# Optimization experiments

Hardware: AMD Instinct MI355X
Metric: run time of the kernel (lower is better)

The kernel has to match this reference:

```python
import jax, jax.numpy as jnp
import numpy as np

N = 50000        # nodes
E = 800000       # directed edges (before self-loops)
NODE_DIM = 128
HIDDEN = 64
HEADS = 4
C = HIDDEN // HEADS   # 16 per-head channels
LAYERS = 4
G = 256          # graphs in batch
EPS = 1e-5       # BatchNorm eps
SLOPE = 0.2      # GAT leaky_relu negative slope


def setup_inputs() -> dict:
    key = jax.random.key(0)
    ks = jax.random.split(key, 12)

    def gl(k, shape, fan_in):  # glorot-ish init
        return jax.random.normal(k, shape, jnp.float32) * np.float32(1.0 / np.sqrt(fan_in))

    x = jax.random.normal(ks[0], (N, NODE_DIM), jnp.float32)
    edge_index = jax.random.randint(ks[1], (2, E), 0, N)
    batch = jnp.sort(jax.random.randint(ks[2], (N,), 0, G))

    return {
        "x": x,
        "embed_W": gl(ks[3], (NODE_DIM, HIDDEN), NODE_DIM),
        "embed_b": jnp.zeros((HIDDEN,), jnp.float32),
        "gat_W": gl(ks[4], (LAYERS, HIDDEN, HIDDEN), HIDDEN),
        "att_src": gl(ks[5], (LAYERS, HEADS, C), C),
        "att_dst": gl(ks[6], (LAYERS, HEADS, C), C),
        "gat_b": jnp.zeros((LAYERS, HIDDEN), jnp.float32),
        "bn_gamma": jnp.ones((LAYERS, HIDDEN), jnp.float32),
        "bn_beta": jnp.zeros((LAYERS, HIDDEN), jnp.float32),
        "fc1_W": gl(ks[7], (HIDDEN, HIDDEN), HIDDEN),
        "fc1_b": jnp.zeros((HIDDEN,), jnp.float32),
        "fc2_W": gl(ks[8], (HIDDEN, 1), HIDDEN),
        "fc2_b": jnp.zeros((1,), jnp.float32),
        "edge_index": edge_index,
        "batch": batch,
    }


def reference(x, embed_W, embed_b, gat_W, att_src, att_dst, gat_b,
              bn_gamma, bn_beta, fc1_W, fc1_b, fc2_W, fc2_b,
              edge_index, batch):
    # GATConv default: add self-loops (message flows src -> dst)
    loops = jnp.arange(N)
    src = jnp.concatenate([edge_index[0], loops])
    dst = jnp.concatenate([edge_index[1], loops])

    h = x @ embed_W + embed_b  # [N, HIDDEN]
    for l in range(LAYERS):
        xp = (h @ gat_W[l]).reshape(N, HEADS, C)          # per-head transform
        a_s = jnp.sum(xp * att_src[l], axis=-1)           # [N, H]
        a_d = jnp.sum(xp * att_dst[l], axis=-1)           # [N, H]
        e = jax.nn.leaky_relu(a_s[src] + a_d[dst], SLOPE) # [E', H]
        # segment softmax over incoming edges of each dst node
        m = jax.ops.segment_max(e, dst, num_segments=N)
        p = jnp.exp(e - m[dst])
        s = jax.ops.segment_sum(p, dst, num_segments=N)
        alpha = p / (s[dst] + 1e-16)                      # [E', H]
        msg = xp[src] * alpha[:, :, None]                 # [E', H, C]
        h = jax.ops.segment_sum(msg, dst, num_segments=N).reshape(N, HIDDEN) + gat_b[l]
        # BatchNorm over nodes (training-mode batch stats, biased variance)
        mu = jnp.mean(h, axis=0)
        var = jnp.var(h, axis=0)
        h = (h - mu) * jax.lax.rsqrt(var + EPS) * bn_gamma[l] + bn_beta[l]
        h = jax.nn.elu(h)

    g = jax.ops.segment_sum(h, batch, num_segments=G)     # global_add_pool
    g = jax.nn.relu(g @ fc1_W + fc1_b)                    # dropout: identity (eval)
    return (g @ fc2_W + fc2_b).reshape(-1)                # [G]
```

## Files before the change

kernel.cpp:

```cpp
#include <hip/hip_runtime.h>

#define N_NODES 50000
#define N_EDGES 800000
#define NODE_DIM 128
#define HIDDEN 64
#define HEADS 4
#define LAYERS 4
#define NGRAPH 256
#define BN_EPS 1e-5f
#define SLOPE 0.2f
#define NTILES 196
#define BN_BLOCKS 256
#define NPW 16

typedef unsigned short u16;
typedef unsigned int   u32;

__device__ __forceinline__ float b2f(u16 v) { return __uint_as_float(((u32)v) << 16); }
__device__ __forceinline__ u16 f2b(float f) {
    u32 u = __float_as_uint(f);
    u32 r = (u + 0x7FFFu + ((u >> 16) & 1u)) >> 16;
    return (u16)r;
}
__device__ __forceinline__ float ld(const void* p, int i, int isf) {
    return isf ? ((const float*)p)[i] : b2f(((const u16*)p)[i]);
}

__global__ void k_mark(u16* out, u16 pat) { out[threadIdx.x] = pat; }

__global__ void k_init(const void* gamma, int* flag, int* cnt) {
    int i = blockIdx.x * 256 + threadIdx.x;
    if (i < N_NODES) cnt[i] = 0;
    if (i == 0) *flag = (((const u32*)gamma)[0] == 0x3F800000u) ? 1 : 0;
}

__global__ void k_count(const int* __restrict__ ei, int* __restrict__ cnt,
                        int* __restrict__ eslot) {
    int e = blockIdx.x * 256 + threadIdx.x;
    if (e >= N_EDGES) return;
    eslot[e] = atomicAdd(&cnt[ei[N_EDGES + e]], 1);
}
__global__ void k_scan1(const int* __restrict__ cnt, int* __restrict__ row_ptr,
                        int* __restrict__ tsum) {
    int b = blockIdx.x, t = threadIdx.x, i = b * 256 + t;
    int c = (i < N_NODES) ? cnt[i] : 0;
    __shared__ int ps[256];
    ps[t] = c;
    __syncthreads();
    for (int off = 1; off < 256; off <<= 1) {
        int v = (t >= off) ? ps[t - off] : 0;
        __syncthreads();
        ps[t] += v;
        __syncthreads();
    }
    if (i < N_NODES) row_ptr[i] = ps[t] - c;
    if (t == 255) tsum[b] = ps[255];
}
__global__ void k_scan3(int* __restrict__ row_ptr, const int* __restrict__ tsum) {
    __shared__ int ps[256];
    int t = threadIdx.x;
    int c = (t < NTILES) ? tsum[t] : 0;
    ps[t] = c;
    __syncthreads();
    for (int off = 1; off < 256; off <<= 1) {
        int v = (t >= off) ? ps[t - off] : 0;
        __syncthreads();
        ps[t] += v;
        __syncthreads();
    }
    int toff_b = (blockIdx.x == 0) ? 0 : ps[blockIdx.x - 1];
    int i = blockIdx.x * 256 + t;
    if (i < N_NODES) row_ptr[i] += toff_b;
    if (i == 0) row_ptr[N_NODES] = N_EDGES;
}
__global__ void k_fill(const int* __restrict__ ei, const int* __restrict__ row_ptr,
                       const int* __restrict__ eslot, int* __restrict__ col) {
    int e = blockIdx.x * 256 + threadIdx.x;
    if (e >= N_EDGES) return;
    col[row_ptr[ei[N_EDGES + e]] + eslot[e]] = ei[e];
}

template<int ISF>
__device__ __forceinline__ void embed_tr_body(const void* __restrict__ x,
                                              const void* __restrict__ W,
                                              const void* __restrict__ b,
                                              const void* __restrict__ W0,
                                              const void* __restrict__ asrc,
                                              const void* __restrict__ adst,
                                              u16* __restrict__ xp16,
                                              float* __restrict__ a_s,
                                              float* __restrict__ a_d,
                                              float* __restrict__ bn_part) {
    int t = threadIdx.x;
    int n0 = blockIdx.x * NPW;
    if (blockIdx.x < BN_BLOCKS) {
        bn_part[blockIdx.x * 128 + t] = 0.f;
        bn_part[blockIdx.x * 128 + 64 + t] = 0.f;
    }
    __shared__ float xs[2][4][NODE_DIM];
    __shared__ float hbuf[NPW][HIDDEN];

    {
        float wreg[NODE_DIM];
#pragma unroll
        for (int k = 0; k < NODE_DIM; k++) wreg[k] = ld(W, k * HIDDEN + t, ISF);
        float bias = ld(b, t, ISF);

        float2 r[4];
#pragma unroll
        for (int i = 0; i < 4; i++) {
            if (ISF) {
                r[i] = ((const float2*)x)[(size_t)(n0 + i) * (NODE_DIM / 2) + t];
            } else {
                u32 v = ((const u32*)x)[(size_t)(n0 + i) * (NODE_DIM / 2) + t];
                r[i] = make_float2(__uint_as_float(v << 16), __uint_as_float(v & 0xFFFF0000u));
            }
        }
#pragma unroll
        for (int i = 0; i < 4; i++) *(float2*)&xs[0][i][2 * t] = r[i];

        for (int g = 0; g < NPW / 4; g++) {
            float2 rn[4];
            if (g + 1 < NPW / 4) {
#pragma unroll
                for (int i = 0; i < 4; i++) {
                    int n = n0 + (g + 1) * 4 + i;
                    if (ISF) {
                        rn[i] = ((const float2*)x)[(size_t)n * (NODE_DIM / 2) + t];
                    } else {
                        u32 v = ((const u32*)x)[(size_t)n * (NODE_DIM / 2) + t];
                        rn[i] = make_float2(__uint_as_float(v << 16),
                                            __uint_as_float(v & 0xFFFF0000u));
                    }
                }
            }
#pragma unroll
            for (int i = 0; i < 4; i++) {
                const float* xr = xs[g & 1][i];
                float a0 = 0.f, a1 = 0.f, a2 = 0.f, a3 = 0.f;
#pragma unroll
                for (int k = 0; k < NODE_DIM; k += 4) {
                    float4 xv = *(const float4*)&xr[k];
                    a0 += xv.x * wreg[k];
                    a1 += xv.y * wreg[k + 1];
                    a2 += xv.z * wreg[k + 2];
                    a3 += xv.w * wreg[k + 3];
                }
                hbuf[g * 4 + i][t] = (a0 + a1) + (a2 + a3) + bias;
            }
            if (g + 1 < NPW / 4) {
#pragma unroll
                for (int i = 0; i < 4; i++) *(float2*)&xs[(g + 1) & 1][i][2 * t] = rn[i];
            }
        }
    }

    float w0[HIDDEN];
#pragma unroll
    for (int k = 0; k < HIDDEN; k++) w0[k] = ld(W0, k * HIDDEN + t, ISF);
    float vsc = ld(asrc, t, ISF);
    float vdc = ld(adst, t, ISF);

#pragma unroll 2
    for (int i = 0; i < NPW; i++) {
        int n = n0 + i;
        const float* hr = hbuf[i];
        float a0 = 0.f, a1 = 0.f, a2 = 0.f, a3 = 0.f;
#pragma unroll
        for (int k = 0; k < HIDDEN; k += 4) {
            float4 xv = *(const float4*)&hr[k];
            a0 += xv.x * w0[k];
            a1 += xv.y * w0[k + 1];
            a2 += xv.z * w0[k + 2];
            a3 += xv.w * w0[k + 3];
        }
        float acc = (a0 + a1) + (a2 + a3);
        xp16[(size_t)n * HIDDEN + t] = f2b(acc);
        float vs = acc * vsc, vd = acc * vdc;
#pragma unroll
        for (int o = 1; o < 16; o <<= 1) {
            vs += __shfl_xor(vs, o, 16);
            vd += __shfl_xor(vd, o, 16);
        }
        if ((t & 15) == 0) {
            a_s[n * HEADS + (t >> 4)] = vs;
            a_d[n * HEADS + (t >> 4)] = vd;
        }
    }
}
__global__ void __launch_bounds__(64)
k_embed_tr(const void* __restrict__ x, const void* __restrict__ W,
           const void* __restrict__ b, const void* __restrict__ W0,
           const void* __restrict__ asrc, const void* __restrict__ adst,
           const int* __restrict__ fl,
           u16* __restrict__ xp16, float* __restrict__ a_s, float* __restrict__ a_d,
           float* __restrict__ bn_part) {
    if (*fl) embed_tr_body<1>(x, W, b, W0, asrc, adst, xp16, a_s, a_d, bn_part);
    else     embed_tr_body<0>(x, W, b, W0, asrc, adst, xp16, a_s, a_d, bn_part);
}

template<int ISF>
__device__ __forceinline__ void transform_body(const float* __restrict__ h,
                                               const void* __restrict__ W,
                                               const void* __restrict__ asrc,
                                               const void* __restrict__ adst, int l,
                                               const float* __restrict__ bnss,
                                               u16* __restrict__ xp16,
                                               float* __restrict__ a_s,
                                               float* __restrict__ a_d,
                                               float* __restrict__ bn_part) {
    int t = threadIdx.x;
    int n0 = blockIdx.x * NPW;
    if (blockIdx.x < BN_BLOCKS) {
        bn_part[blockIdx.x * 128 + t] = 0.f;
        bn_part[blockIdx.x * 128 + 64 + t] = 0.f;
    }
    __shared__ float hsb[2][4][HIDDEN];
    float wreg[HIDDEN];
#pragma unroll
    for (int k = 0; k < HIDDEN; k++) wreg[k] = ld(W, l * HIDDEN * HIDDEN + k * HIDDEN + t, ISF);
    float vsc = ld(asrc, l * HIDDEN + t, ISF);
    float vdc = ld(adst, l * HIDDEN + t, ISF);
    float sc = bnss[t], sh = bnss[64 + t];

    float r[4];
#pragma unroll
    for (int i = 0; i < 4; i++) {
        float v = h[(size_t)(n0 + i) * HIDDEN + t];
        v = v * sc + sh;
        v = v > 0.f ? v : (__expf(v) - 1.f);
        r[i] = v;
    }
#pragma unroll
    for (int i = 0; i < 4; i++) hsb[0][i][t] = r[i];

    for (int g = 0; g < NPW / 4; g++) {
        float rn[4];
        if (g + 1 < NPW / 4) {
#pragma unroll
            for (int i = 0; i < 4; i++)
                rn[i] = h[(size_t)(n0 + (g + 1) * 4 + i) * HIDDEN + t];
        }
#pragma unroll
        for (int i = 0; i < 4; i++) {
            int n = n0 + g * 4 + i;
            const float* hr = hsb[g & 1][i];
            float a0 = 0.f, a1 = 0.f, a2 = 0.f, a3 = 0.f;
#pragma unroll
            for (int k = 0; k < HIDDEN; k += 4) {
                float4 xv = *(const float4*)&hr[k];
                a0 += xv.x * wreg[k];
                a1 += xv.y * wreg[k + 1];
                a2 += xv.z * wreg[k + 2];
                a3 += xv.w * wreg[k + 3];
            }
            float acc = (a0 + a1) + (a2 + a3);
            xp16[(size_t)n * HIDDEN + t] = f2b(acc);
            float vs = acc * vsc, vd = acc * vdc;
#pragma unroll
            for (int o = 1; o < 16; o <<= 1) {
                vs += __shfl_xor(vs, o, 16);
                vd += __shfl_xor(vd, o, 16);
            }
            if ((t & 15) == 0) {
                a_s[n * HEADS + (t >> 4)] = vs;
                a_d[n * HEADS + (t >> 4)] = vd;
            }
        }
        if (g + 1 < NPW / 4) {
#pragma unroll
            for (int i = 0; i < 4; i++) {
                float v = rn[i];
                v = v * sc + sh;
                v = v > 0.f ? v : (__expf(v) - 1.f);
                hsb[(g + 1) & 1][i][t] = v;
            }
        }
    }
}
__global__ void __launch_bounds__(64)
k_transform(const float* __restrict__ h, const void* __restrict__ W,
            const void* __restrict__ asrc, const void* __restrict__ adst,
            const int* __restrict__ fl, int l,
            const float* __restrict__ bnss,
            u16* __restrict__ xp16, float* __restrict__ a_s,
            float* __restrict__ a_d, float* __restrict__ bn_part) {
    if (*fl) transform_body<1>(h, W, asrc, adst, l, bnss, xp16, a_s, a_d, bn_part);
    else     transform_body<0>(h, W, asrc, adst, l, bnss, xp16, a_s, a_d, bn_part);
}

__global__ void __launch_bounds__(256)
k_gather(const int* __restrict__ row_ptr, const int* __restrict__ col,
         const float* __restrict__ a_s, const float* __restrict__ a_d,
         const u16* __restrict__ xp16, float* __restrict__ h,
         float* __restrict__ bn_part) {
    int d = blockIdx.x * 4 + (threadIdx.x >> 6);
    int t = threadIdx.x & 63;
    int hd = t >> 4, l16 = t & 15, hb = hd << 4;
    int beg = row_ptr[d], end = row_ptr[d + 1];
    float ad = a_d[d * HEADS + hd];

    float m = a_s[d * HEADS + hd] + ad;
    m = m > 0.f ? m : SLOPE * m;
    float s = 1.f;
    float acc = b2f(xp16[(size_t)d * HIDDEN + t]);

    for (int j0 = beg; j0 < end; j0 += 16) {
        int jj = j0 + l16;
        int sv = col[jj < end ? jj : end - 1];
        float e = -1e30f;
        if (jj < end) {
            e = a_s[sv * HEADS + hd] + ad;
            e = e > 0.f ? e : SLOPE * e;
        }
        float cm = e;
#pragma unroll
        for (int o = 1; o < 16; o <<= 1) cm = fmaxf(cm, __shfl_xor(cm, o, 16));
        float nm = fmaxf(m, cm);
        float scale = __expf(m - nm);
        float alpha = (jj < end) ? __expf(e - nm) : 0.f;
        float cs = alpha;
#pragma unroll
        for (int o = 1; o < 16; o <<= 1) cs += __shfl_xor(cs, o, 16);
        s = s * scale + cs;
        acc *= scale;
#pragma unroll
        for (int q = 0; q < 16; q++) {
            int   svq = __shfl(sv, q, 64);
            float aq  = __shfl(alpha, hb + q, 64);
            acc += aq * b2f(xp16[(size_t)svq * HIDDEN + t]);
        }
        m = nm;
    }
    float v = acc / (s + 1e-16f);
    h[(size_t)d * HIDDEN + t] = v;

    __shared__ float s1[256];
    __shared__ float s2[256];
    s1[threadIdx.x] = v;
    s2[threadIdx.x] = v * v;
    __syncthreads();
    if (threadIdx.x < 64) {
        float su = s1[t] + s1[64 + t] + s1[128 + t] + s1[192 + t];
        float sq = s2[t] + s2[64 + t] + s2[128 + t] + s2[192 + t];
        float* bp = bn_part + (blockIdx.x & (BN_BLOCKS - 1)) * 128;
        atomicAdd(bp + t, su);
        atomicAdd(bp + 64 + t, sq);
    }
}

__global__ void k_bn_final(const float* __restrict__ bn_part,
                           const void* __restrict__ gamma, const void* __restrict__ beta,
                           const int* __restrict__ fl, int l, float* __restrict__ bnss) {
    int t = threadIdx.x;
    float sum = 0.f, sq = 0.f;
#pragma unroll 8
    for (int b = 0; b < BN_BLOCKS; b++) {
        sum += bn_part[b * 128 + t];
        sq  += bn_part[b * 128 + 64 + t];
    }
    int isf = *fl;
    const float inv_n = 1.f / (float)N_NODES;
    float mu  = sum * inv_n;
    float var = sq * inv_n - mu * mu;
    float sc = rsqrtf(var + BN_EPS) * ld(gamma, l * HIDDEN + t, isf);
    bnss[t]      = sc;
    bnss[64 + t] = ld(beta, l * HIDDEN + t, isf) - mu * sc;
}

__global__ void __launch_bounds__(1024)
k_poolmlp(const float* __restrict__ h, const int* __restrict__ batch,
          const float* __restrict__ bnss,
          const void* __restrict__ W1, const void* __restrict__ b1,
          const void* __restrict__ W2, const void* __restrict__ b2,
          const int* __restrict__ fl, void* __restrict__ out) {
    int gr = blockIdx.x;
    int t = threadIdx.x & 63, w = threadIdx.x >> 6;
    int lo = 0, hi = N_NODES;
    while (lo < hi) { int mid = (lo + hi) >> 1; if (batch[mid] < gr) lo = mid + 1; else hi = mid; }
    int beg = lo;
    lo = 0; hi = N_NODES;
    while (lo < hi) { int mid = (lo + hi) >> 1; if (batch[mid] < gr + 1) lo = mid + 1; else hi = mid; }
    int end = lo;
    float sc = bnss[t], sh = bnss[64 + t];
    float acc = 0.f;
    for (int n = beg + w; n < end; n += 16) {
        float v = h[(size_t)n * HIDDEN + t] * sc + sh;
        acc += v > 0.f ? v : (__expf(v) - 1.f);
    }
    __shared__ float sd[1024];
    __shared__ float gs[64];
    sd[threadIdx.x] = acc;
    __syncthreads();
    if (w < 8) sd[threadIdx.x] += sd[threadIdx.x + 512];
    __syncthreads();
    if (w < 4) sd[threadIdx.x] += sd[threadIdx.x + 256];
    __syncthreads();
    if (w < 2) sd[threadIdx.x] += sd[threadIdx.x + 128];
    __syncthreads();
    if (w == 0) gs[t] = sd[t] + sd[t + 64];
    __syncthreads();
    if (w == 0) {
        int isf = *fl;
        float a1 = ld(b1, t, isf);
        for (int k = 0; k < HIDDEN; k++) a1 += gs[k] * ld(W1, k * HIDDEN + t, isf);
        a1 = fmaxf(a1, 0.f);
        float p = a1 * ld(W2, t, isf);
#pragma unroll
        for (int o = 1; o < 64; o <<= 1) p += __shfl_xor(p, o, 64);
        if (t == 0) {
            float r = p + ld(b2, 0, isf);
            if (isf) ((float*)out)[gr] = r;
            else     ((u16*)out)[gr]   = f2b(r);
        }
    }
}

extern "C" void kernel_launch(void* const* d_in, const int* in_sizes, int n_in,
                              void* d_out, int out_size, void* d_ws, size_t ws_size,
                              hipStream_t stream) {
    u16* out16 = (u16*)d_out;

    bool sizes_ok = (n_in == 15) && (out_size == NGRAPH)
        && in_sizes[0] == N_NODES * NODE_DIM
        && in_sizes[1] == NODE_DIM * HIDDEN
        && in_sizes[2] == HIDDEN
        && in_sizes[3] == LAYERS * HIDDEN * HIDDEN
        && in_sizes[4] == LAYERS * HIDDEN
        && in_sizes[5] == LAYERS * HIDDEN
        && in_sizes[6] == LAYERS * HIDDEN
        && in_sizes[7] == LAYERS * HIDDEN
        && in_sizes[8] == LAYERS * HIDDEN
        && in_sizes[9] == HIDDEN * HIDDEN
        && in_sizes[10] == HIDDEN
        && in_sizes[11] == HIDDEN
        && in_sizes[12] == 1
        && in_sizes[13] == 2 * N_EDGES
        && in_sizes[14] == N_NODES;
    if (!sizes_ok) { k_mark<<<1, 256, 0, stream>>>(out16, 0x4442); return; }

    float* ws      = (float*)d_ws;
    float* h       = ws;
    u16*   xp16    = (u16*)(ws + 3200000);
    float* a_s     = ws + 4800000;
    float* a_d     = ws + 5000000;
    float* bn_part = ws + 5200000;
    float* bnss    = ws + 5232768;
    int* row_ptr   = (int*)(ws + 5232896);
    int* cnt       = row_ptr + 50001;
    int* eslot     = cnt + 50000;
    int* col       = eslot + 800000;
    int* tsum      = col + 800000;
    int* dflag     = tsum + 256;

    const size_t NEED_BYTES =
        (size_t)(5232896 + 50001 + 50000 + 800000 + 800000 + 256 + 1) * 4;
    if (ws_size < NEED_BYTES) { k_mark<<<1, 256, 0, stream>>>(out16, 0x447A); return; }

    const void* x        = d_in[0];
    const void* embed_W  = d_in[1];
    const void* embed_b  = d_in[2];
    const void* gat_W    = d_in[3];
    const void* att_src  = d_in[4];
    const void* att_dst  = d_in[5];
    const void* bn_gamma = d_in[7];
    const void* bn_beta  = d_in[8];
    const void* fc1_W    = d_in[9];
    const void* fc1_b    = d_in[10];
    const void* fc2_W    = d_in[11];
    const void* fc2_b    = d_in[12];
    const int* ei        = (const int*)d_in[13];
    const int* batch     = (const int*)d_in[14];

    const int e_blocks = (N_EDGES + 255) / 256;
    k_init<<<(N_NODES + 255) / 256, 256, 0, stream>>>(bn_gamma, dflag, cnt);
    k_count<<<e_blocks, 256, 0, stream>>>(ei, cnt, eslot);
    k_scan1<<<NTILES, 256, 0, stream>>>(cnt, row_ptr, tsum);
    k_scan3<<<NTILES, 256, 0, stream>>>(row_ptr, tsum);
    k_fill<<<e_blocks, 256, 0, stream>>>(ei, row_ptr, eslot, col);

    k_embed_tr<<<N_NODES / NPW, 64, 0, stream>>>(x, embed_W, embed_b, gat_W,
                                                 att_src, att_dst, dflag,
                                                 xp16, a_s, a_d, bn_part);

    for (int l = 0; l < LAYERS; l++) {
        if (l > 0)
            k_transform<<<N_NODES / NPW, 64, 0, stream>>>(h, gat_W, att_src, att_dst,
                                                          dflag, l, bnss,
                                                          xp16, a_s, a_d, bn_part);
        k_gather<<<N_NODES / 4, 256, 0, stream>>>(row_ptr, col, a_s, a_d, xp16, h, bn_part);
        k_bn_final<<<1, 64, 0, stream>>>(bn_part, bn_gamma, bn_beta, dflag, l, bnss);
    }

    k_poolmlp<<<NGRAPH, 1024, 0, stream>>>(h, batch, bnss, fc1_W, fc1_b, fc2_W, fc2_b,
                                           dflag, d_out);
}
```

Measured before the change: 465.8 us.

## Use lane broadcasts instead of LDS for node transforms; fold BN finalize into gather

The embed and transform kernels now keep node feature rows in registers and broadcast each element with readlane instead of staging rows through shared memory. This removes LDS traffic and the related synchronisation. The separate single-block BN finalize kernel is removed: the gather kernel uses an atomic ticket so the last block computes the BN scale and shift. That saves four kernel launches but adds a grid-wide atomic and threadfences, and readlane runs on the scalar path, which may limit throughput.

```diff
diff --git a/kernel.cpp b/kernel.cpp
--- a/kernel.cpp
+++ b/kernel.cpp
@@ -25,6 +25,9 @@
 __device__ __forceinline__ float ld(const void* p, int i, int isf) {
     return isf ? ((const float*)p)[i] : b2f(((const u16*)p)[i]);
 }
+__device__ __forceinline__ float bcast(float v, int l) {
+    return __uint_as_float((u32)__builtin_amdgcn_readlane((int)__float_as_uint(v), l));
+}
 
 __global__ void k_mark(u16* out, u16 pat) { out[threadIdx.x] = pat; }
 
@@ -78,6 +81,16 @@
     int e = blockIdx.x * 256 + threadIdx.x;
     if (e >= N_EDGES) return;
     col[row_ptr[ei[N_EDGES + e]] + eslot[e]] = ei[e];
+}
+
+template<int ISF>
+__device__ __forceinline__ float2 ldx2(const void* x, int n, int t) {
+    if (ISF) {
+        return ((const float2*)x)[(size_t)n * (NODE_DIM / 2) + t];
+    } else {
+        u32 v = ((const u32*)x)[(size_t)n * (NODE_DIM / 2) + t];
+        return make_float2(__uint_as_float(v << 16), __uint_as_float(v & 0xFFFF0000u));
+    }
 }
 
 template<int ISF>
@@ -90,102 +103,69 @@
                                               u16* __restrict__ xp16,
                                               float* __restrict__ a_s,
                                               float* __restrict__ a_d,
-                                              float* __restrict__ bn_part) {
+                                              float* __restrict__ bn_part,
+                                              int* __restrict__ ticket) {
     int t = threadIdx.x;
     int n0 = blockIdx.x * NPW;
     if (blockIdx.x < BN_BLOCKS) {
         bn_part[blockIdx.x * 128 + t] = 0.f;
         bn_part[blockIdx.x * 128 + 64 + t] = 0.f;
-    }
-    __shared__ float xs[2][4][NODE_DIM];
-    __shared__ float hbuf[NPW][HIDDEN];
-
-    {
-        float wreg[NODE_DIM];
-#pragma unroll
-        for (int k = 0; k < NODE_DIM; k++) wreg[k] = ld(W, k * HIDDEN + t, ISF);
-        float bias = ld(b, t, ISF);
-
-        float2 r[4];
-#pragma unroll
-        for (int i = 0; i < 4; i++) {
-            if (ISF) {
-                r[i] = ((const float2*)x)[(size_t)(n0 + i) * (NODE_DIM / 2) + t];
-            } else {
-                u32 v = ((const u32*)x)[(size_t)(n0 + i) * (NODE_DIM / 2) + t];
-                r[i] = make_float2(__uint_as_float(v << 16), __uint_as_float(v & 0xFFFF0000u));
-            }
-        }
-#pragma unroll
-        for (int i = 0; i < 4; i++) *(float2*)&xs[0][i][2 * t] = r[i];
-
-        for (int g = 0; g < NPW / 4; g++) {
-            float2 rn[4];
-            if (g + 1 < NPW / 4) {
-#pragma unroll
-                for (int i = 0; i < 4; i++) {
-                    int n = n0 + (g + 1) * 4 + i;
-                    if (ISF) {
-                        rn[i] = ((const float2*)x)[(size_t)n * (NODE_DIM / 2) + t];
-                    } else {
-                        u32 v = ((const u32*)x)[(size_t)n * (NODE_DIM / 2) + t];
-                        rn[i] = make_float2(__uint_as_float(v << 16),
-                                            __uint_as_float(v & 0xFFFF0000u));
-                    }
-                }
-            }
-#pragma unroll
-            for (int i = 0; i < 4; i++) {
-                const float* xr = xs[g & 1][i];
-                float a0 = 0.f, a1 = 0.f, a2 = 0.f, a3 = 0.f;
-#pragma unroll
-                for (int k = 0; k < NODE_DIM; k += 4) {
-                    float4 xv = *(const float4*)&xr[k];
-                    a0 += xv.x * wreg[k];
-                    a1 += xv.y * wreg[k + 1];
-                    a2 += xv.z * wreg[k + 2];
-                    a3 += xv.w * wreg[k + 3];
-                }
-                hbuf[g * 4 + i][t] = (a0 + a1) + (a2 + a3) + bias;
-            }
-            if (g + 1 < NPW / 4) {
-#pragma unroll
-                for (int i = 0; i < 4; i++) *(float2*)&xs[(g + 1) & 1][i][2 * t] = rn[i];
-            }
-        }
-    }
-
+        if (blockIdx.x == 0 && t == 0) *ticket = 0;
+    }
+    float wreg[NODE_DIM];
+#pragma unroll
+    for (int k = 0; k < NODE_DIM; k++) wreg[k] = ld(W, k * HIDDEN + t, ISF);
     float w0[HIDDEN];
 #pragma unroll
     for (int k = 0; k < HIDDEN; k++) w0[k] = ld(W0, k * HIDDEN + t, ISF);
+    float bias = ld(b, t, ISF);
     float vsc = ld(asrc, t, ISF);
     float vdc = ld(adst, t, ISF);
 
-#pragma unroll 2
-    for (int i = 0; i < NPW; i++) {
-        int n = n0 + i;
-        const float* hr = hbuf[i];
-        float a0 = 0.f, a1 = 0.f, a2 = 0.f, a3 = 0.f;
-#pragma unroll
-        for (int k = 0; k < HIDDEN; k += 4) {
-            float4 xv = *(const float4*)&hr[k];
-            a0 += xv.x * w0[k];
-            a1 += xv.y * w0[k + 1];
-            a2 += xv.z * w0[k + 2];
-            a3 += xv.w * w0[k + 3];
-        }
-        float acc = (a0 + a1) + (a2 + a3);
-        xp16[(size_t)n * HIDDEN + t] = f2b(acc);
-        float vs = acc * vsc, vd = acc * vdc;
-#pragma unroll
-        for (int o = 1; o < 16; o <<= 1) {
-            vs += __shfl_xor(vs, o, 16);
-            vd += __shfl_xor(vd, o, 16);
-        }
-        if ((t & 15) == 0) {
-            a_s[n * HEADS + (t >> 4)] = vs;
-            a_d[n * HEADS + (t >> 4)] = vd;
-        }
+    float2 r[4], rn[4];
+#pragma unroll
+    for (int i = 0; i < 4; i++) r[i] = ldx2<ISF>(x, n0 + i, t);
+
+    for (int g = 0; g < NPW / 4; g++) {
+        if (g + 1 < NPW / 4) {
+#pragma unroll
+            for (int i = 0; i < 4; i++) rn[i] = ldx2<ISF>(x, n0 + (g + 1) * 4 + i, t);
+        }
+#pragma unroll
+        for (int i = 0; i < 4; i++) {
+            int n = n0 + g * 4 + i;
+            float a0 = 0.f, a1 = 0.f, a2 = 0.f, a3 = 0.f;
+#pragma unroll
+            for (int j = 0; j < 64; j += 2) {
+                a0 = fmaf(bcast(r[i].x, j),     wreg[2 * j],     a0);
+                a1 = fmaf(bcast(r[i].y, j),     wreg[2 * j + 1], a1);
+                a2 = fmaf(bcast(r[i].x, j + 1), wreg[2 * j + 2], a2);
+                a3 = fmaf(bcast(r[i].y, j + 1), wreg[2 * j + 3], a3);
+            }
+            float hv = (a0 + a1) + (a2 + a3) + bias;
+            float c0 = 0.f, c1 = 0.f, c2 = 0.f, c3 = 0.f;
+#pragma unroll
+            for (int j = 0; j < HIDDEN; j += 4) {
+                c0 = fmaf(bcast(hv, j),     w0[j],     c0);
+                c1 = fmaf(bcast(hv, j + 1), w0[j + 1], c1);
+                c2 = fmaf(bcast(hv, j + 2), w0[j + 2], c2);
+                c3 = fmaf(bcast(hv, j + 3), w0[j + 3], c3);
+            }
+            float acc = (c0 + c1) + (c2 + c3);
+            xp16[(size_t)n * HIDDEN + t] = f2b(acc);
+            float vs = acc * vsc, vd = acc * vdc;
+#pragma unroll
+            for (int o = 1; o < 16; o <<= 1) {
+                vs += __shfl_xor(vs, o, 16);
+                vd += __shfl_xor(vd, o, 16);
+            }
+            if ((t & 15) == 0) {
+                a_s[n * HEADS + (t >> 4)] = vs;
+                a_d[n * HEADS + (t >> 4)] = vd;
+            }
+        }
+#pragma unroll
+        for (int i = 0; i < 4; i++) r[i] = rn[i];
     }
 }
 __global__ void __launch_bounds__(64)
@@ -194,9 +174,9 @@
            const void* __restrict__ asrc, const void* __restrict__ adst,
            const int* __restrict__ fl,
            u16* __restrict__ xp16, float* __restrict__ a_s, float* __restrict__ a_d,
-           float* __restrict__ bn_part) {
-    if (*fl) embed_tr_body<1>(x, W, b, W0, asrc, adst, xp16, a_s, a_d, bn_part);
-    else     embed_tr_body<0>(x, W, b, W0, asrc, adst, xp16, a_s, a_d, bn_part);
+           float* __restrict__ bn_part, int* __restrict__ ticket) {
+    if (*fl) embed_tr_body<1>(x, W, b, W0, asrc, adst, xp16, a_s, a_d, bn_part, ticket);
+    else     embed_tr_body<0>(x, W, b, W0, asrc, adst, xp16, a_s, a_d, bn_part, ticket);
 }
 
 template<int ISF>
@@ -208,14 +188,15 @@
                                                u16* __restrict__ xp16,
                                                float* __restrict__ a_s,
                                                float* __restrict__ a_d,
-                                               float* __restrict__ bn_part) {
+                                               float* __restrict__ bn_part,
+                                               int* __restrict__ ticket) {
     int t = threadIdx.x;
     int n0 = blockIdx.x * NPW;
     if (blockIdx.x < BN_BLOCKS) {
         bn_part[blockIdx.x * 128 + t] = 0.f;
         bn_part[blockIdx.x * 128 + 64 + t] = 0.f;
-    }
-    __shared__ float hsb[2][4][HIDDEN];
+        if (blockIdx.x == 0 && t == 0) *ticket = 0;
+    }
     float wreg[HIDDEN];
 #pragma unroll
     for (int k = 0; k < HIDDEN; k++) wreg[k] = ld(W, l * HIDDEN * HIDDEN + k * HIDDEN + t, ISF);
@@ -223,38 +204,32 @@
     float vdc = ld(adst, l * HIDDEN + t, ISF);
     float sc = bnss[t], sh = bnss[64 + t];
 
-    float r[4];
+    float v[4], vn[4];
 #pragma unroll
     for (int i = 0; i < 4; i++) {
-        float v = h[(size_t)(n0 + i) * HIDDEN + t];
-        v = v * sc + sh;
-        v = v > 0.f ? v : (__expf(v) - 1.f);
-        r[i] = v;
-    }
-#pragma unroll
-    for (int i = 0; i < 4; i++) hsb[0][i][t] = r[i];
+        float u = h[(size_t)(n0 + i) * HIDDEN + t];
+        u = u * sc + sh;
+        v[i] = u > 0.f ? u : (__expf(u) - 1.f);
+    }
 
     for (int g = 0; g < NPW / 4; g++) {
-        float rn[4];
         if (g + 1 < NPW / 4) {
 #pragma unroll
             for (int i = 0; i < 4; i++)
-                rn[i] = h[(size_t)(n0 + (g + 1) * 4 + i) * HIDDEN + t];
+                vn[i] = h[(size_t)(n0 + (g + 1) * 4 + i) * HIDDEN + t];
         }
 #pragma unroll
         for (int i = 0; i < 4; i++) {
             int n = n0 + g * 4 + i;
-            const float* hr = hsb[g & 1][i];
-            float a0 = 0.f, a1 = 0.f, a2 = 0.f, a3 = 0.f;
-#pragma unroll
-            for (int k = 0; k < HIDDEN; k += 4) {
-                float4 xv = *(const float4*)&hr[k];
-                a0 += xv.x * wreg[k];
-                a1 += xv.y * wreg[k + 1];
-                a2 += xv.z * wreg[k + 2];
-                a3 += xv.w * wreg[k + 3];
-            }
-            float acc = (a0 + a1) + (a2 + a3);
+            float c0 = 0.f, c1 = 0.f, c2 = 0.f, c3 = 0.f;
+#pragma unroll
+            for (int j = 0; j < HIDDEN; j += 4) {
+                c0 = fmaf(bcast(v[i], j),     wreg[j],     c0);
+                c1 = fmaf(bcast(v[i], j + 1), wreg[j + 1], c1);
+                c2 = fmaf(bcast(v[i], j + 2), wreg[j + 2], c2);
+                c3 = fmaf(bcast(v[i], j + 3), wreg[j + 3], c3);
+            }
+            float acc = (c0 + c1) + (c2 + c3);
             xp16[(size_t)n * HIDDEN + t] = f2b(acc);
             float vs = acc * vsc, vd = acc * vdc;
 #pragma unroll
@@ -270,10 +245,8 @@
         if (g + 1 < NPW / 4) {
 #pragma unroll
             for (int i = 0; i < 4; i++) {
-                float v = rn[i];
-                v = v * sc + sh;
-                v = v > 0.f ? v : (__expf(v) - 1.f);
-                hsb[(g + 1) & 1][i][t] = v;
+                float u = vn[i] * sc + sh;
+                v[i] = u > 0.f ? u : (__expf(u) - 1.f);
             }
         }
     }
@@ -284,16 +257,19 @@
             const int* __restrict__ fl, int l,
             const float* __restrict__ bnss,
             u16* __restrict__ xp16, float* __restrict__ a_s,
-            float* __restrict__ a_d, float* __restrict__ bn_part) {
-    if (*fl) transform_body<1>(h, W, asrc, adst, l, bnss, xp16, a_s, a_d, bn_part);
-    else     transform_body<0>(h, W, asrc, adst, l, bnss, xp16, a_s, a_d, bn_part);
+            float* __restrict__ a_d, float* __restrict__ bn_part,
+            int* __restrict__ ticket) {
+    if (*fl) transform_body<1>(h, W, asrc, adst, l, bnss, xp16, a_s, a_d, bn_part, ticket);
+    else     transform_body<0>(h, W, asrc, adst, l, bnss, xp16, a_s, a_d, bn_part, ticket);
 }
 
 __global__ void __launch_bounds__(256)
 k_gather(const int* __restrict__ row_ptr, const int* __restrict__ col,
          const float* __restrict__ a_s, const float* __restrict__ a_d,
          const u16* __restrict__ xp16, float* __restrict__ h,
-         float* __restrict__ bn_part) {
+         float* __restrict__ bn_part, int* __restrict__ ticket,
+         const void* __restrict__ gamma, const void* __restrict__ beta,
+         const int* __restrict__ fl, int l, float* __restrict__ bnss) {
     int d = blockIdx.x * 4 + (threadIdx.x >> 6);
     int t = threadIdx.x & 63;
     int hd = t >> 4, l16 = t & 15, hb = hd << 4;
@@ -337,6 +313,7 @@
 
     __shared__ float s1[256];
     __shared__ float s2[256];
+    __shared__ int lastBlk;
     s1[threadIdx.x] = v;
     s2[threadIdx.x] = v * v;
     __syncthreads();
@@ -347,25 +324,27 @@
         atomicAdd(bp + t, su);
         atomicAdd(bp + 64 + t, sq);
     }
-}
-
-__global__ void k_bn_final(const float* __restrict__ bn_part,
-                           const void* __restrict__ gamma, const void* __restrict__ beta,
-                           const int* __restrict__ fl, int l, float* __restrict__ bnss) {
-    int t = threadIdx.x;
-    float sum = 0.f, sq = 0.f;
+    if (threadIdx.x == 0) {
+        __threadfence();
+        lastBlk = (atomicAdd(ticket, 1) == (int)gridDim.x - 1);
+    }
+    __syncthreads();
+    if (lastBlk && threadIdx.x < 64) {
+        __threadfence();
+        float sum = 0.f, sq = 0.f;
 #pragma unroll 8
-    for (int b = 0; b < BN_BLOCKS; b++) {
-        sum += bn_part[b * 128 + t];
-        sq  += bn_part[b * 128 + 64 + t];
-    }
-    int isf = *fl;
-    const float inv_n = 1.f / (float)N_NODES;
-    float mu  = sum * inv_n;
-    float var = sq * inv_n - mu * mu;
-    float sc = rsqrtf(var + BN_EPS) * ld(gamma, l * HIDDEN + t, isf);
-    bnss[t]      = sc;
-    bnss[64 + t] = ld(beta, l * HIDDEN + t, isf) - mu * sc;
+        for (int bb = 0; bb < BN_BLOCKS; bb++) {
+            sum += bn_part[bb * 128 + t];
+            sq  += bn_part[bb * 128 + 64 + t];
+        }
+        int isf = *fl;
+        const float inv_n = 1.f / (float)N_NODES;
+        float mu  = sum * inv_n;
+        float var = sq * inv_n - mu * mu;
+        float scl = rsqrtf(var + BN_EPS) * ld(gamma, l * HIDDEN + t, isf);
+        bnss[t]      = scl;
+        bnss[64 + t] = ld(beta, l * HIDDEN + t, isf) - mu * scl;
+    }
 }
 
 __global__ void __launch_bounds__(1024)
@@ -452,9 +431,10 @@
     int* col       = eslot + 800000;
     int* tsum      = col + 800000;
     int* dflag     = tsum + 256;
+    int* ticket    = dflag + 1;
 
     const size_t NEED_BYTES =
-        (size_t)(5232896 + 50001 + 50000 + 800000 + 800000 + 256 + 1) * 4;
+        (size_t)(5232896 + 50001 + 50000 + 800000 + 800000 + 256 + 2) * 4;
     if (ws_size < NEED_BYTES) { k_mark<<<1, 256, 0, stream>>>(out16, 0x447A); return; }
 
     const void* x        = d_in[0];
@@ -481,15 +461,16 @@
 
     k_embed_tr<<<N_NODES / NPW, 64, 0, stream>>>(x, embed_W, embed_b, gat_W,
                                                  att_src, att_dst, dflag,
-                                                 xp16, a_s, a_d, bn_part);
+                                                 xp16, a_s, a_d, bn_part, ticket);
 
     for (int l = 0; l < LAYERS; l++) {
         if (l > 0)
             k_transform<<<N_NODES / NPW, 64, 0, stream>>>(h, gat_W, att_src, att_dst,
                                                           dflag, l, bnss,
-                                                          xp16, a_s, a_d, bn_part);
-        k_gather<<<N_NODES / 4, 256, 0, stream>>>(row_ptr, col, a_s, a_d, xp16, h, bn_part);
-        k_bn_final<<<1, 64, 0, stream>>>(bn_part, bn_gamma, bn_beta, dflag, l, bnss);
+                                                          xp16, a_s, a_d, bn_part, ticket);
+        k_gather<<<N_NODES / 4, 256, 0, stream>>>(row_ptr, col, a_s, a_d, xp16, h,
+                                                  bn_part, ticket,
+                                                  bn_gamma, bn_beta, dflag, l, bnss);
     }
 
     k_poolmlp<<<NGRAPH, 1024, 0, stream>>>(h, batch, bnss, fc1_W, fc1_b, fc2_W, fc2_b,
```

Result: slower. 1.731 ms (+271.6%).
